# Optimization experiments

Measured on AMD Instinct MI355X. Metric: run time of the kernel, lower is better.

## Reference

```python
import jax, jax.numpy as jnp
import numpy as np

HIDDEN = 2048
N_HEADS = 16
N_KV = 4
HEAD_DIM = 128
EPS = 1e-6
B = 8
L = 1024
PREFIX = 256
SUFFIX = L - PREFIX
N_COMPACT = PREFIX + B * SUFFIX  # 6400
T_FULL = B * L                   # 8192
ROPE_THETA = 10000.0


def _radix_indices():
    # full position (b, p) -> compact index
    scatter = np.empty(T_FULL, dtype=np.int64)
    for b in range(B):
        scatter[b * L: b * L + PREFIX] = np.arange(PREFIX)
        scatter[b * L + PREFIX: (b + 1) * L] = PREFIX + b * SUFFIX + np.arange(SUFFIX)
    # compact index -> first full occurrence
    fold = np.empty(N_COMPACT, dtype=np.int64)
    fold[:PREFIX] = np.arange(PREFIX)
    for b in range(B):
        fold[PREFIX + b * SUFFIX: PREFIX + (b + 1) * SUFFIX] = b * L + PREFIX + np.arange(SUFFIX)
    return scatter, fold


def setup_inputs() -> dict:
    key = jax.random.key(0)
    ks = jax.random.split(key, 8)
    scatter_np, fold_np = _radix_indices()
    # per-compact-token positions for RoPE
    pos = np.empty(N_COMPACT, dtype=np.float32)
    pos[:PREFIX] = np.arange(PREFIX)
    for b in range(B):
        pos[PREFIX + b * SUFFIX: PREFIX + (b + 1) * SUFFIX] = PREFIX + np.arange(SUFFIX)
    inv_freq = ROPE_THETA ** (-np.arange(HEAD_DIM // 2, dtype=np.float32) / (HEAD_DIM // 2))
    freqs = pos[:, None] * inv_freq[None, :]  # [N_c, 64]
    s = 0.02
    return {
        "hidden_states": jax.random.normal(ks[0], (N_COMPACT, HIDDEN), jnp.float32),
        "cos": jnp.asarray(np.cos(freqs), jnp.float32),
        "sin": jnp.asarray(np.sin(freqs), jnp.float32),
        "cu_seq_lengths": jnp.arange(B + 1, dtype=jnp.int32) * L,
        "max_seq_len": L,
        "fold_gather": jnp.asarray(fold_np),
        "scatter_indices": jnp.asarray(scatter_np),
        "wq": jax.random.normal(ks[1], (HIDDEN, N_HEADS * HEAD_DIM), jnp.float32) * s,
        "wk": jax.random.normal(ks[2], (HIDDEN, N_KV * HEAD_DIM), jnp.float32) * s,
        "wv": jax.random.normal(ks[3], (HIDDEN, N_KV * HEAD_DIM), jnp.float32) * s,
        "wo": jax.random.normal(ks[4], (N_HEADS * HEAD_DIM, HIDDEN), jnp.float32) * s,
        "q_norm_w": jnp.ones((HEAD_DIM,), jnp.float32),
        "k_norm_w": jnp.ones((HEAD_DIM,), jnp.float32),
    }


def _rmsnorm(x, w):
    xf = x.astype(jnp.float32)
    var = jnp.mean(xf * xf, axis=-1, keepdims=True)
    return (w * (xf * jax.lax.rsqrt(var + EPS))).astype(x.dtype)


def _rope(x, cos, sin):
    # x: [N, H, D]; cos/sin: [N, D/2]
    half = cos.shape[-1]
    x1, x2 = x[..., :half], x[..., half:2 * half]
    c, s = cos[:, None, :], sin[:, None, :]
    return jnp.concatenate([x1 * c - x2 * s, x1 * s + x2 * c], axis=-1)


def reference(hidden_states, cos, sin, cu_seq_lengths, max_seq_len,
              fold_gather, scatter_indices, wq, wk, wv, wo, q_norm_w, k_norm_w):
    N = hidden_states.shape[0]
    q = (hidden_states @ wq).reshape(N, N_HEADS, HEAD_DIM)
    k = (hidden_states @ wk).reshape(N, N_KV, HEAD_DIM)
    v = (hidden_states @ wv).reshape(N, N_KV, HEAD_DIM)
    q = _rope(_rmsnorm(q, q_norm_w), cos, sin)
    k = _rope(_rmsnorm(k, k_norm_w), cos, sin)
    # radix scatter: expand compact tokens to full varlen token stream
    qf = q[scatter_indices].reshape(B, L, N_HEADS, HEAD_DIM)
    kf = k[scatter_indices].reshape(B, L, N_KV, HEAD_DIM)
    vf = v[scatter_indices].reshape(B, L, N_KV, HEAD_DIM)
    group = N_HEADS // N_KV
    kf = jnp.repeat(kf, group, axis=2)
    vf = jnp.repeat(vf, group, axis=2)
    scale = HEAD_DIM ** -0.5
    scores = jnp.einsum('bqhd,bkhd->bhqk', qf, kf) * scale
    causal = jnp.tril(jnp.ones((L, L), dtype=bool))
    scores = jnp.where(causal[None, None], scores, jnp.finfo(scores.dtype).min)
    probs = jax.nn.softmax(scores, axis=-1)
    out = jnp.einsum('bhqk,bkhd->bqhd', probs, vf).reshape(T_FULL, N_HEADS * HEAD_DIM)
    # radix fold: gather back to compact tokens
    out_compact = out[fold_gather]
    return out_compact @ wo
```

## Files before the change

### kernel.cpp

```cpp
#include <hip/hip_runtime.h>
#include <hip/hip_bf16.h>

typedef __bf16 bf16;
typedef __bf16 bf16x4 __attribute__((ext_vector_type(4)));
typedef __bf16 bf16x8 __attribute__((ext_vector_type(8)));
typedef float f32x4 __attribute__((ext_vector_type(4)));

#define HID 2048
#define NHEADS 16
#define NKV 4
#define HD 128
#define NC 6400
#define KVW (NKV * HD)

__device__ __forceinline__ void async_cp16(const bf16* src, bf16* dst_lds) {
  __builtin_amdgcn_global_load_lds(
      (const __attribute__((address_space(1))) void*)src,
      (__attribute__((address_space(3))) void*)dst_lds, 16, 0, 0);
}

__device__ __forceinline__ void xcd_swizzle(int& bx, int& by) {
  int nx = gridDim.x;
  int nwg = nx * gridDim.y;
  int id = by * nx + bx;
  int q = nwg >> 3, r = nwg & 7;
  int xcd = id & 7, idx = id >> 3;
  int nid = (xcd < r ? xcd * (q + 1) : r * (q + 1) + (xcd - r) * q) + idx;
  bx = nid % nx;
  by = nid / nx;
}

__global__ __launch_bounds__(256) void k_cvt(const float* __restrict__ in,
                                             bf16* __restrict__ out) {
  size_t i = ((size_t)blockIdx.x * 256 + threadIdx.x) * 8;
  f32x4 a = *(const f32x4*)(in + i);
  f32x4 b = *(const f32x4*)(in + i + 4);
  bf16x8 t;
  for (int j = 0; j < 4; j++) {
    t[j] = (bf16)a[j];
    t[j + 4] = (bf16)b[j];
  }
  *(bf16x8*)(out + i) = t;
}

__global__ __launch_bounds__(256) void k_transpose(const float* __restrict__ in,
                                                   bf16* __restrict__ out,
                                                   int R, int C) {
  __shared__ bf16 tile[32][33];
  int bc = blockIdx.x * 32, br = blockIdx.y * 32;
  int tx = threadIdx.x & 31, ty = threadIdx.x >> 5;
  for (int i = 0; i < 32; i += 8)
    tile[ty + i][tx] = (bf16)in[(size_t)(br + ty + i) * C + bc + tx];
  __syncthreads();
  for (int i = 0; i < 32; i += 8)
    out[(size_t)(bc + ty + i) * R + br + tx] = tile[tx][ty + i];
}

__device__ __forceinline__ void gemm256_core(
    const bf16* __restrict__ A, const bf16* __restrict__ Bt, int m0, int nloc,
    int K, bf16* AsB, bf16* BsB, f32x4 (&acc)[2][4][4]) {
  const int tid = threadIdx.x;
  const int lane = tid & 63, wave = tid >> 6;
  const int l15 = lane & 15, quad = lane >> 4;
  const int wr = wave >> 2, wc = wave & 3;
  const int r0A = wr * 128 + l15;
  const int r0B = wc * 64 + l15;
  const int colOff0 = (quad * 8) ^ ((l15 & 7) << 3);
  const int colOff1 = (32 + quad * 8) ^ ((l15 & 7) << 3);
  const size_t offS0 =
      (size_t)(tid >> 3) * K + ((((tid & 7) ^ ((tid >> 3) & 7)) << 4) >> 1);
  const size_t offS1 = offS0 + (size_t)64 * K;
  const int dstW0 = wave * 512;
  const int dstW1 = 4096 + wave * 512;
  const bf16* Abase = A + (size_t)m0 * K;
  const bf16* Bbase = Bt + (size_t)nloc * K;
  const int KM = K - 1;

#define STAGE(gb, lds, dbuf, h, kc)                             \
  do {                                                          \
    const bf16* _s = (gb) + (size_t)(h) * 128 * K + (kc);       \
    bf16* _d = (lds) + (dbuf) * 16384 + (h) * 8192;             \
    async_cp16(_s + offS0, _d + dstW0);                         \
    async_cp16(_s + offS1, _d + dstW1);                         \
  } while (0)

#define LDA(dbuf, mh)                                           \
  do {                                                          \
    _Pragma("unroll") for (int i = 0; i < 4; i++) {             \
      int r = r0A + (mh) * 64 + i * 16;                         \
      const bf16* p = AsB + (dbuf) * 16384 + r * 64;            \
      a[i][0] = *(const bf16x8*)(p + colOff0);                  \
      a[i][1] = *(const bf16x8*)(p + colOff1);                  \
    }                                                           \
  } while (0)

#define LDB(dbuf, nh, bb)                                       \
  do {                                                          \
    _Pragma("unroll") for (int j = 0; j < 2; j++) {             \
      int r = r0B + (nh) * 32 + j * 16;                         \
      const bf16* p = BsB + (dbuf) * 16384 + r * 64;            \
      bb[j][0] = *(const bf16x8*)(p + colOff0);                 \
      bb[j][1] = *(const bf16x8*)(p + colOff1);                 \
    }                                                           \
  } while (0)

#define MFMAQ(mh, nh, bb)                                                    \
  do {                                                                       \
    __builtin_amdgcn_s_setprio(1);                                           \
    _Pragma("unroll") for (int i = 0; i < 4; i++)                            \
        _Pragma("unroll") for (int j = 0; j < 2; j++) {                      \
      acc[mh][i][(nh) * 2 + j] = __builtin_amdgcn_mfma_f32_16x16x32_bf16(    \
          a[i][0], bb[j][0], acc[mh][i][(nh) * 2 + j], 0, 0, 0);             \
      acc[mh][i][(nh) * 2 + j] = __builtin_amdgcn_mfma_f32_16x16x32_bf16(    \
          a[i][1], bb[j][1], acc[mh][i][(nh) * 2 + j], 0, 0, 0);             \
    }                                                                        \
    __builtin_amdgcn_s_setprio(0);                                           \
  } while (0)

  STAGE(Abase, AsB, 0, 0, 0);
  STAGE(Abase, AsB, 0, 1, 0);
  STAGE(Bbase, BsB, 0, 0, 0);
  STAGE(Bbase, BsB, 0, 1, 0);
  STAGE(Bbase, BsB, 1, 0, 64);
  STAGE(Bbase, BsB, 1, 1, 64);
  STAGE(Abase, AsB, 1, 0, 64);
  asm volatile("s_waitcnt vmcnt(6)" ::: "memory");
  __builtin_amdgcn_s_barrier();

  bf16x8 a[4][2], b0[2][2], b1[2][2];

  const int NIT = K >> 7;
#pragma unroll 1
  for (int it = 0; it < NIT; ++it) {
    const int kb = it << 7;
    LDA(0, 0);
    LDB(0, 0, b0);
    STAGE(Abase, AsB, 1, 1, (kb + 64) & KM);
    asm volatile("s_waitcnt lgkmcnt(8)");
    __builtin_amdgcn_s_barrier();
    asm volatile("s_waitcnt lgkmcnt(0)" ::: "memory");
    MFMAQ(0, 0, b0);
    __builtin_amdgcn_s_barrier();
    LDB(0, 1, b1);
    __builtin_amdgcn_s_barrier();
    asm volatile("s_waitcnt lgkmcnt(0)" ::: "memory");
    MFMAQ(0, 1, b1);
    __builtin_amdgcn_s_barrier();
    LDA(0, 1);
    STAGE(Bbase, BsB, 0, 0, (kb + 128) & KM);
    __builtin_amdgcn_s_barrier();
    asm volatile("s_waitcnt lgkmcnt(0)" ::: "memory");
    MFMAQ(1, 0, b0);
    __builtin_amdgcn_s_barrier();
    STAGE(Bbase, BsB, 0, 1, (kb + 128) & KM);
    __builtin_amdgcn_s_barrier();
    asm volatile("s_waitcnt lgkmcnt(0)" ::: "memory");
    MFMAQ(1, 1, b1);
    asm volatile("s_waitcnt vmcnt(4)" ::: "memory");
    __builtin_amdgcn_s_barrier();
    LDA(1, 0);
    LDB(1, 0, b0);
    STAGE(Abase, AsB, 0, 0, (kb + 128) & KM);
    asm volatile("s_waitcnt lgkmcnt(8)");
    __builtin_amdgcn_s_barrier();
    asm volatile("s_waitcnt lgkmcnt(0)" ::: "memory");
    MFMAQ(0, 0, b0);
    __builtin_amdgcn_s_barrier();
    LDB(1, 1, b1);
    STAGE(Abase, AsB, 0, 1, (kb + 128) & KM);
    __builtin_amdgcn_s_barrier();
    asm volatile("s_waitcnt lgkmcnt(0)" ::: "memory");
    MFMAQ(0, 1, b1);
    __builtin_amdgcn_s_barrier();
    LDA(1, 1);
    STAGE(Bbase, BsB, 1, 0, (kb + 192) & KM);
    __builtin_amdgcn_s_barrier();
    asm volatile("s_waitcnt lgkmcnt(0)" ::: "memory");
    MFMAQ(1, 0, b0);
    __builtin_amdgcn_s_barrier();
    STAGE(Bbase, BsB, 1, 1, (kb + 192) & KM);
    STAGE(Abase, AsB, 1, 0, (kb + 192) & KM);
    __builtin_amdgcn_s_barrier();
    asm volatile("s_waitcnt lgkmcnt(0)" ::: "memory");
    MFMAQ(1, 1, b1);
    asm volatile("s_waitcnt vmcnt(6)" ::: "memory");
    __builtin_amdgcn_s_barrier();
  }
#undef STAGE
#undef LDA
#undef LDB
#undef MFMAQ
}

__global__ __launch_bounds__(512, 2) void k_proj(const bf16* __restrict__ A,
                                                 const bf16* __restrict__ wqT,
                                                 const bf16* __restrict__ wkT,
                                                 const bf16* __restrict__ wvT,
                                                 bf16* __restrict__ qb,
                                                 bf16* __restrict__ kb,
                                                 bf16* __restrict__ vtb) {
  __shared__ __align__(16) bf16 smem[2][2][256][64];
  int bx = blockIdx.x, by = blockIdx.y;
  xcd_swizzle(bx, by);
  int n0 = bx * 256, m0 = by * 256;

  const bf16* bt;
  int nloc, outsel;
  if (n0 < HID) {
    bt = wqT; nloc = n0; outsel = 0;
  } else if (n0 < HID + KVW) {
    bt = wkT; nloc = n0 - HID; outsel = 1;
  } else {
    bt = wvT; nloc = n0 - HID - KVW; outsel = 2;
  }

  const f32x4 fz = {0.0f, 0.0f, 0.0f, 0.0f};
  f32x4 acc[2][4][4];
#pragma unroll
  for (int mh = 0; mh < 2; mh++)
#pragma unroll
    for (int i = 0; i < 4; i++)
#pragma unroll
      for (int j = 0; j < 4; j++) acc[mh][i][j] = fz;

  gemm256_core(A, bt, m0, nloc, HID, &smem[0][0][0][0], &smem[1][0][0][0], acc);

  int tid = threadIdx.x, lane = tid & 63, wave = tid >> 6;
  int l15 = lane & 15, quad = lane >> 4;
  int wr = wave >> 2, wc = wave & 3;

  if (outsel == 2) {
    asm volatile("s_waitcnt vmcnt(0)" ::: "memory");
    __syncthreads();
    bf16* sm = &smem[0][0][0][0];
#pragma unroll
    for (int mh = 0; mh < 2; mh++)
#pragma unroll
      for (int i = 0; i < 4; i++)
#pragma unroll
        for (int nj = 0; nj < 4; nj++) {
          int col = wc * 64 + nj * 16 + l15;
          int row = wr * 128 + mh * 64 + i * 16 + quad * 4;
          int idx = col * 256 + ((row + ((col & 7) << 3)) & 255);
          bf16x4 v4 = {(bf16)acc[mh][i][nj][0], (bf16)acc[mh][i][nj][1],
                       (bf16)acc[mh][i][nj][2], (bf16)acc[mh][i][nj][3]};
          *(bf16x4*)&sm[idx] = v4;
        }
    __syncthreads();
#pragma unroll
    for (int p = 0; p < 4; p++) {
      int cc = p * 64 + (tid >> 3);
      int h = tid & 7;
#pragma unroll
      for (int j = 0; j < 4; j++) {
        int row8 = h * 32 + j * 8;
        bf16x8 v =
            *(const bf16x8*)&sm[cc * 256 + ((row8 + ((cc & 7) << 3)) & 255)];
        *(bf16x8*)(vtb + (size_t)(nloc + cc) * NC + m0 + row8) = v;
      }
    }
  } else {
#pragma unroll
    for (int mh = 0; mh < 2; mh++)
#pragma unroll
      for (int i = 0; i < 4; i++)
#pragma unroll
        for (int nj = 0; nj < 4; nj++)
#pragma unroll
          for (int r = 0; r < 4; r++) {
            int row = m0 + wr * 128 + mh * 64 + i * 16 + quad * 4 + r;
            int col = nloc + wc * 64 + nj * 16 + l15;
            float v = acc[mh][i][nj][r];
            if (outsel == 0)
              qb[(size_t)row * HID + col] = (bf16)v;
            else
              kb[(size_t)row * KVW + col] = (bf16)v;
          }
  }
}

__global__ __launch_bounds__(512, 2) void k_gemm_out(const bf16* __restrict__ A,
                                                     const bf16* __restrict__ Bt,
                                                     float* __restrict__ C,
                                                     int M, int N, int K) {
  __shared__ __align__(16) bf16 smem[2][2][256][64];
  int bx = blockIdx.x, by = blockIdx.y;
  xcd_swizzle(bx, by);
  int n0 = bx * 256, m0 = by * 256;

  const f32x4 fz = {0.0f, 0.0f, 0.0f, 0.0f};
  f32x4 acc[2][4][4];
#pragma unroll
  for (int mh = 0; mh < 2; mh++)
#pragma unroll
    for (int i = 0; i < 4; i++)
#pragma unroll
      for (int j = 0; j < 4; j++) acc[mh][i][j] = fz;

  gemm256_core(A, Bt, m0, n0, K, &smem[0][0][0][0], &smem[1][0][0][0], acc);

  int tid = threadIdx.x, lane = tid & 63, wave = tid >> 6;
  int l15 = lane & 15, quad = lane >> 4;
  int wr = wave >> 2, wc = wave & 3;
#pragma unroll
  for (int mh = 0; mh < 2; mh++)
#pragma unroll
    for (int i = 0; i < 4; i++)
#pragma unroll
      for (int nj = 0; nj < 4; nj++)
#pragma unroll
        for (int r = 0; r < 4; r++) {
          int row = m0 + wr * 128 + mh * 64 + i * 16 + quad * 4 + r;
          int col = n0 + wc * 64 + nj * 16 + l15;
          C[(size_t)row * N + col] = acc[mh][i][nj][r];
        }
}

__global__ __launch_bounds__(256) void k_normrope(bf16* __restrict__ q,
                                                  bf16* __restrict__ k,
                                                  const float* __restrict__ cs,
                                                  const float* __restrict__ sn,
                                                  const float* __restrict__ qw,
                                                  const float* __restrict__ kw) {
  int pair = blockIdx.x * 4 + (threadIdx.x >> 6);
  int lane = threadIdx.x & 63;
  int n = pair / 20, hh = pair % 20;
  bf16* base;
  const float* w;
  if (hh < 16) {
    base = q + (size_t)n * HID + hh * HD;
    w = qw;
  } else {
    base = k + (size_t)n * KVW + (hh - 16) * HD;
    w = kw;
  }
  float x1 = (float)base[lane], x2 = (float)base[lane + 64];
  float ss = x1 * x1 + x2 * x2;
  for (int o = 32; o; o >>= 1) ss += __shfl_xor(ss, o);
  float inv = rsqrtf(ss * (1.0f / 128.0f) + 1e-6f);
  float x1n = x1 * inv * w[lane];
  float x2n = x2 * inv * w[lane + 64];
  float c = cs[(size_t)n * 64 + lane];
  float s = sn[(size_t)n * 64 + lane];
  base[lane] = (bf16)(x1n * c - x2n * s);
  base[lane + 64] = (bf16)(x1n * s + x2n * c);
}

__global__ __launch_bounds__(256) void k_attn(const bf16* __restrict__ qb,
                                              const bf16* __restrict__ kb,
                                              const bf16* __restrict__ vt,
                                              bf16* __restrict__ ob) {
  int t = blockIdx.x;
  int h = blockIdx.y;
  int kh = h >> 2;
  int tid = threadIdx.x;
  int lane = tid & 63, wave = tid >> 6;
  int l15 = lane & 15, quad = lane >> 4;

  int b, p0, nbase;
  if (t < 96) {
    int ti = 11 - (t >> 3);
    b = t & 7;
    p0 = 256 + ti * 64;
    nbase = 256 + b * 768 + ti * 64;
  } else {
    int pt = 99 - t;
    b = 0;
    p0 = pt * 64;
    nbase = pt * 64;
  }

  __shared__ __align__(16) bf16 Ks[2][64][128];
  __shared__ __align__(16) bf16 Vs[2][128][64];
  __shared__ __align__(16) bf16 Ps[4][16][72];

#define STAGE_KV(buf, kbase)                                                  \
  do {                                                                        \
    _Pragma("unroll") for (int i = 0; i < 4; i++) {                           \
      int rowK = wave * 16 + i * 4 + quad;                                    \
      async_cp16(kb + (size_t)((kbase) + rowK) * KVW + kh * HD +              \
                     ((l15 ^ ((i * 4 + quad) & 7)) << 3),                     \
                 &Ks[buf][0][0] + (wave * 4 + i) * 512);                      \
    }                                                                         \
    _Pragma("unroll") for (int i = 0; i < 4; i++) {                           \
      int dV = wave * 32 + i * 8 + (lane >> 3);                               \
      async_cp16(vt + (size_t)(kh * HD + dV) * NC + (kbase) +                 \
                     (((lane & 7) ^ (lane >> 3)) << 3),                       \
                 &Vs[buf][0][0] + (wave * 4 + i) * 512);                      \
    }                                                                         \
  } while (0)

  bf16x8 aq[4];
  {
    const bf16* qp =
        qb + (size_t)(nbase + wave * 16 + l15) * HID + h * HD + quad * 8;
#pragma unroll
    for (int ks = 0; ks < 4; ks++) aq[ks] = *(const bf16x8*)(qp + ks * 32);
  }
  int qpos[4];
#pragma unroll
  for (int r = 0; r < 4; r++) qpos[r] = p0 + wave * 16 + quad * 4 + r;

  const f32x4 fz = {0.0f, 0.0f, 0.0f, 0.0f};
  f32x4 oacc[8];
#pragma unroll
  for (int i = 0; i < 8; i++) oacc[i] = fz;
  float mrow[4], lrow[4];
#pragma unroll
  for (int r = 0; r < 4; r++) {
    mrow[r] = -3.0e38f;
    lrow[r] = 0.0f;
  }
  const float scale = 0.08838834764831845f;
  const int swzc = (l15 & 7) << 3;

  int nkt = p0 / 64 + 1;

  STAGE_KV(0, 0);
  asm volatile("s_waitcnt vmcnt(0)" ::: "memory");
  __syncthreads();

  int cur = 0;
  for (int kt = 0; kt < nkt; kt++) {
    int kpos0 = kt * 64;
    bool hasnext = (kt + 1 < nkt);
    if (hasnext) {
      int kposN = kpos0 + 64;
      int kbaseN = (kposN < 256) ? kposN : 256 + b * 768 + (kposN - 256);
      STAGE_KV(cur ^ 1, kbaseN);
      __builtin_amdgcn_sched_barrier(0);
    }

    bool diag = (kt == nkt - 1);
    float sv[4][4];
#pragma unroll
    for (int nt = 0; nt < 4; nt++) {
      f32x4 z = fz;
      __builtin_amdgcn_s_setprio(1);
#pragma unroll
      for (int ks = 0; ks < 4; ks++) {
        bf16x8 kf =
            *(const bf16x8*)&Ks[cur][nt * 16 + l15][(ks * 32 + quad * 8) ^ swzc];
        z = __builtin_amdgcn_mfma_f32_16x16x32_bf16(aq[ks], kf, z, 0, 0, 0);
      }
      __builtin_amdgcn_s_setprio(0);
      int kpos = kpos0 + nt * 16 + l15;
#pragma unroll
      for (int r = 0; r < 4; r++) {
        float v = z[r] * scale;
        if (diag && kpos > qpos[r]) v = -1.0e30f;
        sv[nt][r] = v;
      }
    }
    float alpha[4];
#pragma unroll
    for (int r = 0; r < 4; r++) {
      float mx = fmaxf(fmaxf(sv[0][r], sv[1][r]), fmaxf(sv[2][r], sv[3][r]));
      for (int o = 1; o < 16; o <<= 1) mx = fmaxf(mx, __shfl_xor(mx, o));
      float mnew = fmaxf(mrow[r], mx);
      alpha[r] = __expf(mrow[r] - mnew);
      mrow[r] = mnew;
      float ps = 0.0f;
#pragma unroll
      for (int nt = 0; nt < 4; nt++) {
        float p = __expf(sv[nt][r] - mnew);
        sv[nt][r] = p;
        ps += p;
      }
      for (int o = 1; o < 16; o <<= 1) ps += __shfl_xor(ps, o);
      lrow[r] = lrow[r] * alpha[r] + ps;
    }
#pragma unroll
    for (int i = 0; i < 8; i++)
#pragma unroll
      for (int r = 0; r < 4; r++) oacc[i][r] *= alpha[r];

#pragma unroll
    for (int nt = 0; nt < 4; nt++)
#pragma unroll
      for (int r = 0; r < 4; r++)
        Ps[wave][quad * 4 + r][nt * 16 + l15] = (bf16)sv[nt][r];
    asm volatile("s_waitcnt lgkmcnt(0)" ::: "memory");
    bf16x8 pa[2];
#pragma unroll
    for (int ks = 0; ks < 2; ks++)
      pa[ks] = *(const bf16x8*)&Ps[wave][l15][ks * 32 + quad * 8];
    __builtin_amdgcn_s_setprio(1);
#pragma unroll
    for (int dt = 0; dt < 8; dt++)
#pragma unroll
      for (int ks = 0; ks < 2; ks++) {
        bf16x8 vf =
            *(const bf16x8*)&Vs[cur][dt * 16 + l15][(ks * 32 + quad * 8) ^ swzc];
        oacc[dt] =
            __builtin_amdgcn_mfma_f32_16x16x32_bf16(pa[ks], vf, oacc[dt], 0, 0, 0);
      }
    __builtin_amdgcn_s_setprio(0);

    if (hasnext) {
      asm volatile("s_waitcnt vmcnt(0)" ::: "memory");
      __syncthreads();
      cur ^= 1;
    }
  }
#undef STAGE_KV
#pragma unroll
  for (int r = 0; r < 4; r++) {
    float il = 1.0f / lrow[r];
    bf16* op = ob + (size_t)(nbase + wave * 16 + quad * 4 + r) * HID + h * HD;
#pragma unroll
    for (int dt = 0; dt < 8; dt++) op[dt * 16 + l15] = (bf16)(oacc[dt][r] * il);
  }
}

extern "C" void kernel_launch(void* const* d_in, const int* in_sizes, int n_in,
                              void* d_out, int out_size, void* d_ws,
                              size_t ws_size, hipStream_t stream) {
  const float* hs = (const float*)d_in[0];
  const float* cs = (const float*)d_in[1];
  const float* sn = (const float*)d_in[2];
  const float* wq = (const float*)d_in[7];
  const float* wk = (const float*)d_in[8];
  const float* wv = (const float*)d_in[9];
  const float* wo = (const float*)d_in[10];
  const float* qnw = (const float*)d_in[11];
  const float* knw = (const float*)d_in[12];
  float* out = (float*)d_out;

  bf16* hsb = (bf16*)d_out;
  bf16* wqT = hsb + (size_t)NC * HID;
  bf16* wkT = wqT + (size_t)HID * HID;
  bf16* wvT = wkT + (size_t)KVW * HID;
  bf16* qb  = (bf16*)d_in[0];
  bf16* ab  = qb + (size_t)NC * HID;
  bf16* woT = qb;
  bf16* kb  = (bf16*)d_ws;
  bf16* vtb = kb + (size_t)NC * KVW;

  k_cvt<<<dim3(NC * HID / (256 * 8)), 256, 0, stream>>>(hs, hsb);
  k_transpose<<<dim3(HID / 32, HID / 32), 256, 0, stream>>>(wq, wqT, HID, HID);
  k_transpose<<<dim3(KVW / 32, HID / 32), 256, 0, stream>>>(wk, wkT, HID, KVW);
  k_transpose<<<dim3(KVW / 32, HID / 32), 256, 0, stream>>>(wv, wvT, HID, KVW);

  k_proj<<<dim3((HID + 2 * KVW) / 256, NC / 256), 512, 0, stream>>>(
      hsb, wqT, wkT, wvT, qb, kb, vtb);

  k_normrope<<<dim3(NC * 20 / 4), 256, 0, stream>>>(qb, kb, cs, sn, qnw, knw);

  k_attn<<<dim3(100, NHEADS), 256, 0, stream>>>(qb, kb, vtb, ab);

  k_transpose<<<dim3(HID / 32, HID / 32), 256, 0, stream>>>(wo, woT, HID, HID);

  k_gemm_out<<<dim3(HID / 256, NC / 256), 512, 0, stream>>>(ab, woT, out, NC, HID, HID);
}
```

Before: 451.9 us.

## Fold softmax scale into Q, use exp2, and skip rescale via lazy max

Pre-multiplies Q by scale*log2(e) once so the inner loop needs no per-score multiply and can use exp2f. Adds lazy online-softmax rescaling: the running max and the O accumulator rescale are updated only when some row's new max exceeds the old by more than 8 (in log2 units). This removes the per-tile alpha exp and the 32 multiplies. The Ps row padding changes from 72 to 76 to alter the LDS bank mapping. Rounding Q to bf16 after scaling adds a small precision change, and the lazy threshold lets exponentials reach up to 2^8 before renormalising.

```diff
diff --git a/kernel.cpp b/kernel.cpp
--- a/kernel.cpp
+++ b/kernel.cpp
@@ -372,7 +372,7 @@
 
   __shared__ __align__(16) bf16 Ks[2][64][128];
   __shared__ __align__(16) bf16 Vs[2][128][64];
-  __shared__ __align__(16) bf16 Ps[4][16][72];
+  __shared__ __align__(16) bf16 Ps[4][16][76];
 
 #define STAGE_KV(buf, kbase)                                                  \
   do {                                                                        \
@@ -390,12 +390,18 @@
     }                                                                         \
   } while (0)
 
+  const float qscale = 0.08838834764831845f * 1.4426950408889634f;
   bf16x8 aq[4];
   {
     const bf16* qp =
         qb + (size_t)(nbase + wave * 16 + l15) * HID + h * HD + quad * 8;
 #pragma unroll
-    for (int ks = 0; ks < 4; ks++) aq[ks] = *(const bf16x8*)(qp + ks * 32);
+    for (int ks = 0; ks < 4; ks++) {
+      bf16x8 v = *(const bf16x8*)(qp + ks * 32);
+#pragma unroll
+      for (int e = 0; e < 8; e++) v[e] = (bf16)((float)v[e] * qscale);
+      aq[ks] = v;
+    }
   }
   int qpos[4];
 #pragma unroll
@@ -411,7 +417,6 @@
     mrow[r] = -3.0e38f;
     lrow[r] = 0.0f;
   }
-  const float scale = 0.08838834764831845f;
   const int swzc = (l15 & 7) << 3;
 
   int nkt = p0 / 64 + 1;
@@ -444,36 +449,52 @@
         z = __builtin_amdgcn_mfma_f32_16x16x32_bf16(aq[ks], kf, z, 0, 0, 0);
       }
       __builtin_amdgcn_s_setprio(0);
-      int kpos = kpos0 + nt * 16 + l15;
+#pragma unroll
+      for (int r = 0; r < 4; r++) sv[nt][r] = z[r];
+    }
+    if (diag) {
+#pragma unroll
+      for (int nt = 0; nt < 4; nt++) {
+        int kpos = kpos0 + nt * 16 + l15;
+#pragma unroll
+        for (int r = 0; r < 4; r++)
+          if (kpos > qpos[r]) sv[nt][r] = -1.0e30f;
+      }
+    }
+    float mx[4];
+#pragma unroll
+    for (int r = 0; r < 4; r++) {
+      float m = fmaxf(fmaxf(sv[0][r], sv[1][r]), fmaxf(sv[2][r], sv[3][r]));
+#pragma unroll
+      for (int o = 1; o < 16; o <<= 1) m = fmaxf(m, __shfl_xor(m, o));
+      mx[r] = m;
+    }
+    bool ok = (mx[0] <= mrow[0] + 8.0f) && (mx[1] <= mrow[1] + 8.0f) &&
+              (mx[2] <= mrow[2] + 8.0f) && (mx[3] <= mrow[3] + 8.0f);
+    if (!__all(ok)) {
 #pragma unroll
       for (int r = 0; r < 4; r++) {
-        float v = z[r] * scale;
-        if (diag && kpos > qpos[r]) v = -1.0e30f;
-        sv[nt][r] = v;
+        float mnew = fmaxf(mrow[r], mx[r]);
+        float alpha = exp2f(mrow[r] - mnew);
+        mrow[r] = mnew;
+        lrow[r] *= alpha;
+#pragma unroll
+        for (int i = 0; i < 8; i++) oacc[i][r] *= alpha;
       }
     }
-    float alpha[4];
 #pragma unroll
     for (int r = 0; r < 4; r++) {
-      float mx = fmaxf(fmaxf(sv[0][r], sv[1][r]), fmaxf(sv[2][r], sv[3][r]));
-      for (int o = 1; o < 16; o <<= 1) mx = fmaxf(mx, __shfl_xor(mx, o));
-      float mnew = fmaxf(mrow[r], mx);
-      alpha[r] = __expf(mrow[r] - mnew);
-      mrow[r] = mnew;
       float ps = 0.0f;
 #pragma unroll
       for (int nt = 0; nt < 4; nt++) {
-        float p = __expf(sv[nt][r] - mnew);
+        float p = exp2f(sv[nt][r] - mrow[r]);
         sv[nt][r] = p;
         ps += p;
       }
+#pragma unroll
       for (int o = 1; o < 16; o <<= 1) ps += __shfl_xor(ps, o);
-      lrow[r] = lrow[r] * alpha[r] + ps;
-    }
-#pragma unroll
-    for (int i = 0; i < 8; i++)
-#pragma unroll
-      for (int r = 0; r < 4; r++) oacc[i][r] *= alpha[r];
+      lrow[r] += ps;
+    }
 
 #pragma unroll
     for (int nt = 0; nt < 4; nt++)
```

New measurement: 457.8 us. No clear change (+1.3%).
